# Kernel tuning notes

Measured on AMD Instinct MI355X. Metric: run time of the kernel, lower is better.

## Reference

```python
import jax, jax.numpy as jnp
import numpy as np

EMBED_DIM = 1024
N_HEAD = 16
D_K = EMBED_DIM // N_HEAD


def setup_inputs() -> dict:
    key = jax.random.key(0)
    kq, kk, kv, kwq, kwk, kwv, kwo = jax.random.split(key, 7)
    B, S, E = 4, 2048, EMBED_DIM
    scale = 1.0 / np.sqrt(E)
    return {
        "Q": jax.random.normal(kq, (B, S, E), dtype=jnp.float32),
        "K": jax.random.normal(kk, (B, S, E), dtype=jnp.float32),
        "V": jax.random.normal(kv, (B, S, E), dtype=jnp.float32),
        "mask": jnp.zeros((1,), dtype=jnp.bool_),  # unused by the module's forward
        "Wq": jax.random.normal(kwq, (E, E), dtype=jnp.float32) * scale,
        "Wk": jax.random.normal(kwk, (E, E), dtype=jnp.float32) * scale,
        "Wv": jax.random.normal(kwv, (E, E), dtype=jnp.float32) * scale,
        "Wo": jax.random.normal(kwo, (E, E), dtype=jnp.float32) * scale,
    }


def reference(Q, K, V, mask, Wq, Wk, Wv, Wo):
    B, S, E = Q.shape
    H, Dk = N_HEAD, D_K
    # Linear projections (torch Linear: x @ W.T), split into heads -> [B,H,S,Dk]
    q = (Q @ Wq.T).reshape(B, S, H, Dk).transpose(0, 2, 1, 3)
    k = (K @ Wk.T).reshape(B, S, H, Dk).transpose(0, 2, 1, 3)
    v = (V @ Wv.T).reshape(B, S, H, Dk).transpose(0, 2, 1, 3)
    # Scaled dot-product attention (no mask is passed in the original forward;
    # dropout is identity in eval mode)
    scores = jnp.einsum("bhqd,bhkd->bhqk", q, k) / jnp.sqrt(jnp.float32(Dk))
    attn = jax.nn.softmax(scores, axis=-1)
    ctx = jnp.einsum("bhqk,bhkd->bhqd", attn, v)  # [B,H,S,Dk]
    ctx = ctx.transpose(0, 2, 1, 3).reshape(B, S, E)
    return ctx @ Wo.T
```

## Files before the change

kernel.cpp:

```cpp
#include <hip/hip_runtime.h>
#include <hip/hip_bf16.h>

#define B_  4
#define S_  2048
#define E_  1024
#define H_  16
#define DK_ 64
#define CSC 0.18033688011112042f

using bf16   = __bf16;
using bf16x8 = __attribute__((ext_vector_type(8))) __bf16;
using f32x4  = __attribute__((ext_vector_type(4))) float;

__device__ __forceinline__ f32x4 mfma16(bf16x8 a, bf16x8 b, f32x4 c) {
    return __builtin_amdgcn_mfma_f32_16x16x32_bf16(a, b, c, 0, 0, 0);
}

__device__ __forceinline__ bf16x8 cvt8(float4 a, float4 b) {
    bf16x8 r;
    r[0] = (bf16)a.x; r[1] = (bf16)a.y; r[2] = (bf16)a.z; r[3] = (bf16)a.w;
    r[4] = (bf16)b.x; r[5] = (bf16)b.y; r[6] = (bf16)b.z; r[7] = (bf16)b.w;
    return r;
}

__device__ __forceinline__ void gl16(const void* g, void* l) {
    __builtin_amdgcn_global_load_lds(
        (const __attribute__((address_space(1))) void*)g,
        (__attribute__((address_space(3))) void*)l, 16, 0, 0);
}

__global__ __launch_bounds__(256) void cvtw3(const float* __restrict__ a,
                                             const float* __restrict__ b,
                                             const float* __restrict__ c,
                                             bf16* __restrict__ d) {
    const int y = blockIdx.y;
    const float* s = y == 0 ? a : y == 1 ? b : c;
    const size_t i = (size_t)blockIdx.x * 256 + threadIdx.x;
    const float4 u = ((const float4*)s)[i * 2];
    const float4 v = ((const float4*)s)[i * 2 + 1];
    ((bf16x8*)(d + (size_t)y * E_ * E_))[i] = cvt8(u, v);
}

__global__ __launch_bounds__(256, 3) void gemm_qkv(
    const float* __restrict__ Qi, const float* __restrict__ Ki,
    const float* __restrict__ Vi, const bf16* __restrict__ Wb,
    bf16* __restrict__ qws, bf16* __restrict__ kws, bf16* __restrict__ vtws) {
    __shared__ __align__(16) float sA[128 * 32];
    __shared__ __align__(16) bf16  sB[128 * 32];

    const int t = threadIdx.x;
    const int lane = t & 63, wave = t >> 6;
    const int wm = wave >> 1, wn = wave & 1;
    const int quad = lane >> 4, l16 = lane & 15;

    const int sel = blockIdx.y >> 3;
    const int gm = blockIdx.x * 128;
    const int gn = (blockIdx.y & 7) * 128;

    const float* A = sel == 0 ? Qi : sel == 1 ? Ki : Vi;
    const bf16* W = Wb + (size_t)sel * E_ * E_;

    const int arow = lane >> 3;
    const int acg  = (lane & 7) ^ (arow & 7);
    const float* gA[4];
#pragma unroll
    for (int j = 0; j < 4; ++j)
        gA[j] = A + (size_t)(gm + wave * 32 + j * 8 + arow) * E_ + acg * 4;

    const int brow = lane >> 2;
    const int bcg  = (lane & 3) ^ ((lane >> 3) & 3);
    const bf16* gB[2];
#pragma unroll
    for (int j = 0; j < 2; ++j)
        gB[j] = W + (size_t)(gn + wave * 32 + j * 16 + brow) * E_ + bcg * 8;

    f32x4 acc[4][4];
#pragma unroll
    for (int i = 0; i < 4; ++i)
#pragma unroll
        for (int j = 0; j < 4; ++j) acc[i][j] = f32x4{0.f, 0.f, 0.f, 0.f};

    for (int kt = 0; kt < E_ / 32; ++kt) {
        __syncthreads();
#pragma unroll
        for (int j = 0; j < 4; ++j)
            gl16(gA[j] + kt * 32, (char*)sA + (wave * 4 + j) * 1024);
#pragma unroll
        for (int j = 0; j < 2; ++j)
            gl16(gB[j] + kt * 32, (char*)sB + (wave * 2 + j) * 1024);
        __syncthreads();

        bf16x8 Af[4], Bf[4];
#pragma unroll
        for (int ms = 0; ms < 4; ++ms) {
            const int r = wm * 64 + ms * 16 + l16, sw = r & 7;
            const float4 a0 = *(const float4*)((const char*)sA + r * 128 +
                                               (((quad * 2) ^ sw) * 16));
            const float4 a1 = *(const float4*)((const char*)sA + r * 128 +
                                               (((quad * 2 + 1) ^ sw) * 16));
            Af[ms] = cvt8(a0, a1);
        }
#pragma unroll
        for (int ns = 0; ns < 4; ++ns) {
            const int r = wn * 64 + ns * 16 + l16;
            Bf[ns] = *(const bf16x8*)((const char*)sB + r * 64 +
                                      ((quad ^ ((r >> 1) & 3)) * 16));
        }
#pragma unroll
        for (int ms = 0; ms < 4; ++ms)
#pragma unroll
            for (int ns = 0; ns < 4; ++ns)
                acc[ms][ns] = mfma16(Af[ms], Bf[ns], acc[ms][ns]);
    }

#pragma unroll
    for (int ms = 0; ms < 4; ++ms)
#pragma unroll
        for (int ns = 0; ns < 4; ++ns) {
            const int col = gn + wn * 64 + ns * 16 + l16;
            const int row0 = gm + wm * 64 + ms * 16 + quad * 4;
            const int h = col >> 6, d = col & (DK_ - 1);
#pragma unroll
            for (int r = 0; r < 4; ++r) {
                const int i = row0 + r;
                const int bb = i >> 11, s = i & (S_ - 1);
                float v = acc[ms][ns][r];
                if (sel == 0) v *= CSC;
                if (sel == 2)
                    vtws[(((size_t)(bb * H_ + h)) * DK_ + d) * S_ + s] = (bf16)v;
                else if (sel == 1)
                    kws[(((size_t)(bb * H_ + h)) * S_ + s) * DK_ + d] = (bf16)v;
                else
                    qws[(((size_t)(bb * H_ + h)) * S_ + s) * DK_ + d] = (bf16)v;
            }
        }
}

__global__ __launch_bounds__(256, 3) void gemm_out(const bf16* __restrict__ A,
                                                   const bf16* __restrict__ W,
                                                   float* __restrict__ out) {
    __shared__ __align__(16) bf16 sA[128 * 32];
    __shared__ __align__(16) bf16 sB[128 * 32];

    const int t = threadIdx.x;
    const int lane = t & 63, wave = t >> 6;
    const int wm = wave >> 1, wn = wave & 1;
    const int quad = lane >> 4, l16 = lane & 15;
    const int gm = blockIdx.x * 128;
    const int gn = blockIdx.y * 128;

    const int brow = lane >> 2;
    const int bcg  = (lane & 3) ^ ((lane >> 3) & 3);
    const bf16* gA[2];
    const bf16* gB[2];
#pragma unroll
    for (int j = 0; j < 2; ++j) {
        gA[j] = A + (size_t)(gm + wave * 32 + j * 16 + brow) * E_ + bcg * 8;
        gB[j] = W + (size_t)(gn + wave * 32 + j * 16 + brow) * E_ + bcg * 8;
    }

    f32x4 acc[4][4];
#pragma unroll
    for (int i = 0; i < 4; ++i)
#pragma unroll
        for (int j = 0; j < 4; ++j) acc[i][j] = f32x4{0.f, 0.f, 0.f, 0.f};

    for (int kt = 0; kt < E_ / 32; ++kt) {
        __syncthreads();
#pragma unroll
        for (int j = 0; j < 2; ++j) {
            gl16(gA[j] + kt * 32, (char*)sA + (wave * 2 + j) * 1024);
            gl16(gB[j] + kt * 32, (char*)sB + (wave * 2 + j) * 1024);
        }
        __syncthreads();

        bf16x8 Af[4], Bf[4];
#pragma unroll
        for (int ms = 0; ms < 4; ++ms) {
            const int r = wm * 64 + ms * 16 + l16;
            Af[ms] = *(const bf16x8*)((const char*)sA + r * 64 +
                                      ((quad ^ ((r >> 1) & 3)) * 16));
        }
#pragma unroll
        for (int ns = 0; ns < 4; ++ns) {
            const int r = wn * 64 + ns * 16 + l16;
            Bf[ns] = *(const bf16x8*)((const char*)sB + r * 64 +
                                      ((quad ^ ((r >> 1) & 3)) * 16));
        }
#pragma unroll
        for (int ms = 0; ms < 4; ++ms)
#pragma unroll
            for (int ns = 0; ns < 4; ++ns)
                acc[ms][ns] = mfma16(Af[ms], Bf[ns], acc[ms][ns]);
    }

#pragma unroll
    for (int ms = 0; ms < 4; ++ms)
#pragma unroll
        for (int ns = 0; ns < 4; ++ns) {
            const int col = gn + wn * 64 + ns * 16 + l16;
            const int row0 = gm + wm * 64 + ms * 16 + quad * 4;
#pragma unroll
            for (int r = 0; r < 4; ++r)
                out[(size_t)(row0 + r) * E_ + col] = acc[ms][ns][r];
        }
}

#define PSTR 72
__global__ __launch_bounds__(256) void attn4(const bf16* __restrict__ q,
                                             const bf16* __restrict__ k,
                                             const bf16* __restrict__ vt,
                                             bf16* __restrict__ ctx) {
    __shared__ __align__(16) bf16 sK[64 * 64];
    __shared__ __align__(16) bf16 sV[64 * 64];
    __shared__ __align__(16) bf16 plds[4][32 * PSTR];

    const int t = threadIdx.x;
    const int lane = t & 63, wave = t >> 6;
    const int quad = lane >> 4, l16 = lane & 15;
    const int qb = (blockIdx.x * 4 + wave) * 32;
    const int bh = blockIdx.y;
    const size_t base  = (size_t)bh * S_ * DK_;
    const size_t baseT = (size_t)bh * DK_ * S_;
    bf16* pw = &plds[wave][0];

    const int srow = t >> 2, sc4 = (t & 3) * 16;
    const int cb = (t & 3) * 2, swr = srow & 7;
    const bf16* gK = k + base + (size_t)srow * DK_ + sc4;
    const bf16* gV = vt + baseT + (size_t)srow * S_ + sc4;
    char* wK0 = (char*)sK + srow * 128 + ((cb ^ swr) * 16);
    char* wK1 = (char*)sK + srow * 128 + (((cb + 1) ^ swr) * 16);
    char* wV0 = (char*)sV + srow * 128 + ((cb ^ swr) * 16);
    char* wV1 = (char*)sV + srow * 128 + (((cb + 1) ^ swr) * 16);

    bf16x8 rk[2], rv[2];
    rk[0] = *(const bf16x8*)(gK);
    rk[1] = *(const bf16x8*)(gK + 8);
    rv[0] = *(const bf16x8*)(gV);
    rv[1] = *(const bf16x8*)(gV + 8);

    bf16x8 aQ[2][2];
#pragma unroll
    for (int t2 = 0; t2 < 2; ++t2) {
        const bf16* qp = q + base + (size_t)(qb + t2 * 16 + l16) * DK_ + quad * 8;
        aQ[t2][0] = *(const bf16x8*)(qp);
        aQ[t2][1] = *(const bf16x8*)(qp + 32);
    }

    f32x4 acc[2][4];
    float l_i[2][4];
#pragma unroll
    for (int t2 = 0; t2 < 2; ++t2)
#pragma unroll
        for (int nb = 0; nb < 4; ++nb) {
            acc[t2][nb] = f32x4{0.f, 0.f, 0.f, 0.f};
            l_i[t2][nb] = 0.f;
        }

    for (int kt = 0; kt < S_ / 64; ++kt) {
        __syncthreads();
        *(bf16x8*)wK0 = rk[0];
        *(bf16x8*)wK1 = rk[1];
        *(bf16x8*)wV0 = rv[0];
        *(bf16x8*)wV1 = rv[1];
        __syncthreads();
        if (kt + 1 < S_ / 64) {
            const bf16* nK = gK + (size_t)(kt + 1) * 64 * DK_;
            const bf16* nV = gV + (size_t)(kt + 1) * 64;
            rk[0] = *(const bf16x8*)(nK);
            rk[1] = *(const bf16x8*)(nK + 8);
            rv[0] = *(const bf16x8*)(nV);
            rv[1] = *(const bf16x8*)(nV + 8);
        }

        f32x4 sc[2][4];
#pragma unroll
        for (int kb = 0; kb < 4; ++kb) {
            const int r = kb * 16 + l16, sw = r & 7;
            const bf16x8 b0 =
                *(const bf16x8*)((const char*)sK + r * 128 + ((quad ^ sw) * 16));
            const bf16x8 b1 = *(const bf16x8*)((const char*)sK + r * 128 +
                                               (((quad + 4) ^ sw) * 16));
#pragma unroll
            for (int t2 = 0; t2 < 2; ++t2) {
                f32x4 z = f32x4{0.f, 0.f, 0.f, 0.f};
                z = mfma16(aQ[t2][0], b0, z);
                sc[t2][kb] = mfma16(aQ[t2][1], b1, z);
            }
        }

#pragma unroll
        for (int t2 = 0; t2 < 2; ++t2)
#pragma unroll
            for (int r = 0; r < 4; ++r) {
                const int prow = (t2 * 16 + quad * 4 + r) * PSTR;
#pragma unroll
                for (int kb = 0; kb < 4; ++kb) {
                    const float p = __builtin_amdgcn_exp2f(sc[t2][kb][r]);
                    l_i[t2][r] += p;
                    pw[prow + kb * 16 + l16] = (bf16)p;
                }
            }

        bf16x8 aP[2][2];
#pragma unroll
        for (int t2 = 0; t2 < 2; ++t2) {
            aP[t2][0] = *(const bf16x8*)(pw + (t2 * 16 + l16) * PSTR + quad * 8);
            aP[t2][1] = *(const bf16x8*)(pw + (t2 * 16 + l16) * PSTR + 32 + quad * 8);
        }

#pragma unroll
        for (int nb = 0; nb < 4; ++nb) {
            const int r = nb * 16 + l16, sw = r & 7;
            const bf16x8 b0 =
                *(const bf16x8*)((const char*)sV + r * 128 + ((quad ^ sw) * 16));
            const bf16x8 b1 = *(const bf16x8*)((const char*)sV + r * 128 +
                                               (((quad + 4) ^ sw) * 16));
#pragma unroll
            for (int t2 = 0; t2 < 2; ++t2) {
                acc[t2][nb] = mfma16(aP[t2][0], b0, acc[t2][nb]);
                acc[t2][nb] = mfma16(aP[t2][1], b1, acc[t2][nb]);
            }
        }
    }

#pragma unroll
    for (int t2 = 0; t2 < 2; ++t2)
#pragma unroll
        for (int r = 0; r < 4; ++r) {
            float x = l_i[t2][r];
            x += __shfl_xor(x, 1);
            x += __shfl_xor(x, 2);
            x += __shfl_xor(x, 4);
            x += __shfl_xor(x, 8);
            l_i[t2][r] = 1.f / x;
        }

    const int b = bh >> 4, h = bh & (H_ - 1);
#pragma unroll
    for (int t2 = 0; t2 < 2; ++t2)
#pragma unroll
        for (int nb = 0; nb < 4; ++nb)
#pragma unroll
            for (int r = 0; r < 4; ++r) {
                const int s = qb + t2 * 16 + quad * 4 + r;
                const size_t idx =
                    ((size_t)(b * S_ + s)) * E_ + h * DK_ + nb * 16 + l16;
                ctx[idx] = (bf16)(acc[t2][nb][r] * l_i[t2][r]);
            }
}

extern "C" void kernel_launch(void* const* d_in, const int* in_sizes, int n_in,
                              void* d_out, int out_size, void* d_ws,
                              size_t ws_size, hipStream_t stream) {
    const float* Q  = (const float*)d_in[0];
    const float* K  = (const float*)d_in[1];
    const float* V  = (const float*)d_in[2];
    const float* Wq = (const float*)d_in[4];
    const float* Wk = (const float*)d_in[5];
    const float* Wv = (const float*)d_in[6];
    const float* Wo = (const float*)d_in[7];
    float* out = (float*)d_out;

    const size_t NTOK = (size_t)B_ * S_ * E_;
    bf16* qws  = (bf16*)d_ws;
    bf16* kws  = qws + NTOK;
    bf16* vtws = kws + NTOK;
    bf16* cws  = vtws + NTOK;

    bf16* wqkvb = cws;
    bf16* wob   = qws;

    const int CW_BLK = E_ * E_ / 8 / 256;

    cvtw3<<<dim3(CW_BLK, 3), 256, 0, stream>>>(Wq, Wk, Wv, wqkvb);

    gemm_qkv<<<dim3(B_ * S_ / 128, 24), 256, 0, stream>>>(
        Q, K, V, Wq ? wqkvb : wqkvb, qws, kws, vtws);

    attn4<<<dim3(S_ / 128, B_ * H_), 256, 0, stream>>>(qws, kws, vtws, cws);

    cvtw3<<<dim3(CW_BLK, 1), 256, 0, stream>>>(Wo, Wo, Wo, wob);

    gemm_out<<<dim3(B_ * S_ / 128, E_ / 128), 256, 0, stream>>>(cws, wob, out);
}
```

Before: 382.5 us.

## Register-prefetch and convert activations to bf16 before LDS in QKV GEMM

The QKV projection GEMM now loads fp32 activation tiles into registers one k-step ahead, converts them to bf16, and stores bf16 into a swizzled LDS tile. This halves LDS footprint and read traffic for A and replaces the direct global-to-LDS fp32 copy. The Q scaling constant is folded into the Wq bf16 conversion instead of the epilogue, and launch bounds are raised to 6 blocks per CU for both GEMMs. Folding the scale into weights before the bf16 rounding slightly changes numerics, and the register prefetch adds VGPR pressure against the higher occupancy target.

Measured after the change: 843.4 us. 120% more time.

```diff
diff --git a/kernel.cpp b/kernel.cpp
--- a/kernel.cpp
+++ b/kernel.cpp
@@ -32,21 +32,24 @@
 __global__ __launch_bounds__(256) void cvtw3(const float* __restrict__ a,
                                              const float* __restrict__ b,
                                              const float* __restrict__ c,
-                                             bf16* __restrict__ d) {
+                                             bf16* __restrict__ d, float s0) {
     const int y = blockIdx.y;
     const float* s = y == 0 ? a : y == 1 ? b : c;
+    const float sc = y == 0 ? s0 : 1.f;
     const size_t i = (size_t)blockIdx.x * 256 + threadIdx.x;
-    const float4 u = ((const float4*)s)[i * 2];
-    const float4 v = ((const float4*)s)[i * 2 + 1];
+    float4 u = ((const float4*)s)[i * 2];
+    float4 v = ((const float4*)s)[i * 2 + 1];
+    u.x *= sc; u.y *= sc; u.z *= sc; u.w *= sc;
+    v.x *= sc; v.y *= sc; v.z *= sc; v.w *= sc;
     ((bf16x8*)(d + (size_t)y * E_ * E_))[i] = cvt8(u, v);
 }
 
-__global__ __launch_bounds__(256, 3) void gemm_qkv(
+__global__ __launch_bounds__(256, 6) void gemm_qkv(
     const float* __restrict__ Qi, const float* __restrict__ Ki,
     const float* __restrict__ Vi, const bf16* __restrict__ Wb,
     bf16* __restrict__ qws, bf16* __restrict__ kws, bf16* __restrict__ vtws) {
-    __shared__ __align__(16) float sA[128 * 32];
-    __shared__ __align__(16) bf16  sB[128 * 32];
+    __shared__ __align__(16) bf16 sA[128 * 32];
+    __shared__ __align__(16) bf16 sB[128 * 32];
 
     const int t = threadIdx.x;
     const int lane = t & 63, wave = t >> 6;
@@ -60,12 +63,11 @@
     const float* A = sel == 0 ? Qi : sel == 1 ? Ki : Vi;
     const bf16* W = Wb + (size_t)sel * E_ * E_;
 
-    const int arow = lane >> 3;
-    const int acg  = (lane & 7) ^ (arow & 7);
-    const float* gA[4];
-#pragma unroll
-    for (int j = 0; j < 4; ++j)
-        gA[j] = A + (size_t)(gm + wave * 32 + j * 8 + arow) * E_ + acg * 4;
+    const int srow = t >> 1, scol = (t & 1) * 16;
+    const float* ga = A + (size_t)(gm + srow) * E_ + scol;
+    const int cb = (t & 1) * 2, swA = (srow >> 1) & 3;
+    bf16* la0 = (bf16*)((char*)sA + srow * 64 + ((cb ^ swA) * 16));
+    bf16* la1 = (bf16*)((char*)sA + srow * 64 + (((cb + 1) ^ swA) * 16));
 
     const int brow = lane >> 2;
     const int bcg  = (lane & 3) ^ ((lane >> 3) & 3);
@@ -74,6 +76,10 @@
     for (int j = 0; j < 2; ++j)
         gB[j] = W + (size_t)(gn + wave * 32 + j * 16 + brow) * E_ + bcg * 8;
 
+    float4 ra[4];
+#pragma unroll
+    for (int j = 0; j < 4; ++j) ra[j] = *(const float4*)(ga + j * 4);
+
     f32x4 acc[4][4];
 #pragma unroll
     for (int i = 0; i < 4; ++i)
@@ -82,23 +88,25 @@
 
     for (int kt = 0; kt < E_ / 32; ++kt) {
         __syncthreads();
-#pragma unroll
-        for (int j = 0; j < 4; ++j)
-            gl16(gA[j] + kt * 32, (char*)sA + (wave * 4 + j) * 1024);
+        *(bf16x8*)la0 = cvt8(ra[0], ra[1]);
+        *(bf16x8*)la1 = cvt8(ra[2], ra[3]);
 #pragma unroll
         for (int j = 0; j < 2; ++j)
             gl16(gB[j] + kt * 32, (char*)sB + (wave * 2 + j) * 1024);
         __syncthreads();
+        if (kt + 1 < E_ / 32) {
+            const int kk = (kt + 1) * 32;
+#pragma unroll
+            for (int j = 0; j < 4; ++j)
+                ra[j] = *(const float4*)(ga + kk + j * 4);
+        }
 
         bf16x8 Af[4], Bf[4];
 #pragma unroll
         for (int ms = 0; ms < 4; ++ms) {
-            const int r = wm * 64 + ms * 16 + l16, sw = r & 7;
-            const float4 a0 = *(const float4*)((const char*)sA + r * 128 +
-                                               (((quad * 2) ^ sw) * 16));
-            const float4 a1 = *(const float4*)((const char*)sA + r * 128 +
-                                               (((quad * 2 + 1) ^ sw) * 16));
-            Af[ms] = cvt8(a0, a1);
+            const int r = wm * 64 + ms * 16 + l16;
+            Af[ms] = *(const bf16x8*)((const char*)sA + r * 64 +
+                                      ((quad ^ ((r >> 1) & 3)) * 16));
         }
 #pragma unroll
         for (int ns = 0; ns < 4; ++ns) {
@@ -124,8 +132,7 @@
             for (int r = 0; r < 4; ++r) {
                 const int i = row0 + r;
                 const int bb = i >> 11, s = i & (S_ - 1);
-                float v = acc[ms][ns][r];
-                if (sel == 0) v *= CSC;
+                const float v = acc[ms][ns][r];
                 if (sel == 2)
                     vtws[(((size_t)(bb * H_ + h)) * DK_ + d) * S_ + s] = (bf16)v;
                 else if (sel == 1)
@@ -136,7 +143,7 @@
         }
 }
 
-__global__ __launch_bounds__(256, 3) void gemm_out(const bf16* __restrict__ A,
+__global__ __launch_bounds__(256, 6) void gemm_out(const bf16* __restrict__ A,
                                                    const bf16* __restrict__ W,
                                                    float* __restrict__ out) {
     __shared__ __align__(16) bf16 sA[128 * 32];
@@ -373,14 +380,14 @@
 
     const int CW_BLK = E_ * E_ / 8 / 256;
 
-    cvtw3<<<dim3(CW_BLK, 3), 256, 0, stream>>>(Wq, Wk, Wv, wqkvb);
+    cvtw3<<<dim3(CW_BLK, 3), 256, 0, stream>>>(Wq, Wk, Wv, wqkvb, CSC);
 
     gemm_qkv<<<dim3(B_ * S_ / 128, 24), 256, 0, stream>>>(
-        Q, K, V, Wq ? wqkvb : wqkvb, qws, kws, vtws);
+        Q, K, V, wqkvb, qws, kws, vtws);
 
     attn4<<<dim3(S_ / 128, B_ * H_), 256, 0, stream>>>(qws, kws, vtws, cws);
 
-    cvtw3<<<dim3(CW_BLK, 1), 256, 0, stream>>>(Wo, Wo, Wo, wob);
+    cvtw3<<<dim3(CW_BLK, 1), 256, 0, stream>>>(Wo, Wo, Wo, wob, 1.f);
 
     gemm_out<<<dim3(B_ * S_ / 128, E_ / 128), 256, 0, stream>>>(cws, wob, out);
 }
```
